# Kernel tuning notes

Hardware: AMD Instinct MI355X
Metric: run time of the kernel (lower is better)

## Reference

```python
import jax, jax.numpy as jnp
import numpy as np

HID = 256
BATCH = 16384
L_K = 4


def _mixture(lst, Ws):
    # lst: [B, 4, H] candidate tensors; Ws: [H] scoring vector (Linear(H,1,bias=False))
    scores = jnp.einsum('bkh,h->bk', lst, Ws)            # [B, 4]
    w = jax.nn.softmax(scores, axis=-1)                  # softmax over the l=4 candidates
    out = jnp.einsum('bk,bkh->bh', w, lst)               # [B, H] mixture
    s = scores.sum(axis=0)                               # [4] summed over batch
    idx = jnp.argmax(s).astype(jnp.int32)                # routing decision
    ss = jnp.sort(s)
    margin = ss[-1] - ss[-2]                             # top-2 margin
    return out, idx, margin


def setup_inputs() -> dict:
    key = jax.random.key(0)
    ks = jax.random.split(key, 6)
    bound = 1.0 / np.sqrt(HID)
    x = jax.random.normal(ks[0], (BATCH, 1, HID), dtype=jnp.float32)
    h = jax.random.normal(ks[1], (BATCH, 1, HID), dtype=jnp.float32)
    L = jax.random.uniform(ks[2], (L_K, HID, HID), dtype=jnp.float32, minval=-bound, maxval=bound)
    R = jax.random.uniform(ks[3], (L_K, HID, HID), dtype=jnp.float32, minval=-bound, maxval=bound)
    # k=3 slots are initialized to identity / zero bias in the torch module
    L = L.at[3].set(jnp.eye(HID, dtype=jnp.float32))
    R = R.at[3].set(jnp.eye(HID, dtype=jnp.float32))
    b = jnp.zeros((L_K, HID), dtype=jnp.float32)
    Ws = jax.random.normal(ks[4], (HID,), dtype=jnp.float32) * bound
    return {'x': x, 'h': h, 'L': L, 'R': R, 'b': b, 'Ws': Ws}


def reference(x, h, L, R, b, Ws):
    x2 = x[:, 0, :]  # [B, H]
    h2 = h[:, 0, :]  # [B, H]

    z1 = jax.nn.sigmoid(x2 @ L[0] + h2 @ R[0] + b[0])
    r = jax.nn.sigmoid(x2 @ L[1] + h2 @ R[1] + b[1])
    z2 = jax.nn.sigmoid(x2 @ L[0] + h2 @ R[0] + b[0])  # identical expression in the source

    def lin(A, Bv):
        # candidate set: A @ L[k] + Bv @ R[k] + b[k] for k in 0..3 -> [B, 4, H]
        return jnp.einsum('bh,khd->bkd', A, L) + jnp.einsum('bh,khd->bkd', Bv, R) + b[None]

    rh, i1, m1 = _mixture(lin(h2, r), Ws)
    h_tilde, i2, m2 = _mixture(lin(x2, rh), Ws)

    omz_cand = 1.0 - (jnp.einsum('bh,khd->bkd', z1, R) + b[None])
    oneMinusZ1, i3, m3 = _mixture(omz_cand, Ws)

    zh_cand = jnp.einsum('bh,khd->bkd', h_tilde, L) * jnp.einsum('bh,khd->bkd', oneMinusZ1, R) + b[None]
    zh_tilde, i4, m4 = _mixture(zh_cand, Ws)

    z2h_cand = jnp.einsum('bh,khd->bkd', h2, L) * jnp.einsum('bh,khd->bkd', z2, R) + b[None]
    z2h, i5, m5 = _mixture(z2h_cand, Ws)

    h_next, i6, m6 = _mixture(lin(zh_tilde, z2h), Ws)

    G_structure = jnp.concatenate([
        jnp.array([0, 1, 0], dtype=jnp.int32),
        jnp.stack([i1, i2, i3, i4, i5, i6]),
    ])
    G_node = jnp.stack([z1, r, z2, rh, h_tilde, oneMinusZ1, zh_tilde, z2h, h_next], axis=1)  # [B, 9, H]
    margins = jnp.stack([m1, m2, m3, m4, m5, m6])
    return h_next[:, None, :], G_structure, G_node, margins
```

## Files before the change

### kernel.cpp

```cpp
#include <hip/hip_runtime.h>

typedef __bf16 bf16_t;
typedef bf16_t bf16x8 __attribute__((ext_vector_type(8)));
typedef float f32x4 __attribute__((ext_vector_type(4)));

#define BATCH 16384
#define HID 256

__device__ __forceinline__ ushort f2b(float f) {
  union { float f; unsigned u; } v; v.f = f;
  unsigned u = v.u;
  unsigned r = (u + 0x7fffu + ((u >> 16) & 1u)) >> 16;
  return (ushort)r;
}
__device__ __forceinline__ float b2f(ushort u) {
  union { unsigned u; float f; } v; v.u = ((unsigned)u) << 16; return v.f;
}
__device__ __forceinline__ void loadbf4(const ushort* __restrict__ p, float* o) {
  uint2 q = *(const uint2*)p;
  o[0] = b2f((ushort)(q.x & 0xffffu));
  o[1] = b2f((ushort)(q.x >> 16));
  o[2] = b2f((ushort)(q.y & 0xffffu));
  o[3] = b2f((ushort)(q.y >> 16));
}
__device__ __forceinline__ uint2 packbf4(const float* v) {
  uint2 q;
  q.x = (unsigned)f2b(v[0]) | ((unsigned)f2b(v[1]) << 16);
  q.y = (unsigned)f2b(v[2]) | ((unsigned)f2b(v[3]) << 16);
  return q;
}

__global__ __launch_bounds__(256)
void f2b2_kernel(const float* __restrict__ a, const float* __restrict__ b,
                 ushort* __restrict__ oa, ushort* __restrict__ ob) {
  int bid = blockIdx.x;
  const float* in = (bid < 4096) ? a : b;
  ushort* out     = (bid < 4096) ? oa : ob;
  int t = (bid & 4095) * 256 + threadIdx.x;
  float4 v = *(const float4*)(in + (size_t)t * 4);
  float q[4] = {v.x, v.y, v.z, v.w};
  *(uint2*)(out + (size_t)t * 4) = packbf4(q);
}

__global__ __launch_bounds__(256)
void wt2_kernel(const float* __restrict__ L, const float* __restrict__ R,
                ushort* __restrict__ Lt, ushort* __restrict__ Rt) {
  int bid = blockIdx.x;
  const float* W = (bid < 1024) ? L : R;
  ushort* Wt     = (bid < 1024) ? Lt : Rt;
  int idx = (bid & 1023) * 256 + threadIdx.x;
  int c = idx >> 8, hh = idx & 255;
  int ks = c >> 8, d = c & 255;
  Wt[idx] = f2b(W[ks * 65536 + hh * 256 + d]);
}

__global__ __launch_bounds__(256, 2)
void gemm_kernel(const ushort* __restrict__ A, const ushort* __restrict__ Wt,
                 ushort* __restrict__ P, int N) {
  __shared__ __align__(16) ushort As[2][128 * 64];
  __shared__ __align__(16) ushort Bs[2][128 * 64];

  const int tid  = threadIdx.x;
  const int lane = tid & 63;
  const int wave = tid >> 6;

  const int nwg = gridDim.x;
  const int q   = nwg >> 3;
  const int bid = blockIdx.x;
  const int id2 = (bid & 7) * q + (bid >> 3);
  const int nx  = N >> 7;
  const int lnx = (nx == 8) ? 3 : 2;
  const int cn  = id2 & (nx - 1);
  const int cm  = id2 >> lnx;
  const int bm  = cm * 128;
  const int bn  = cn * 128;

  const int wm   = (wave >> 1) * 64;
  const int wn   = (wave & 1) * 64;
  const int row  = lane & 15;
  const int quad = lane >> 4;

  const int r_s = lane >> 3;
  const int g_s = lane & 7;
  const int gsw = g_s ^ r_s;

  f32x4 acc[4][4] = {};

#define STAGE(buf, t)                                                              \
  {                                                                                \
    const int k0 = (t) * 64;                                                       \
    for (int i = 0; i < 4; ++i) {                                                  \
      const int ci = wave * 4 + i;                                                 \
      const int r  = ci * 8 + r_s;                                                 \
      const ushort* srcA = A  + (size_t)(bm + r) * 256 + k0 + gsw * 8;             \
      const ushort* srcB = Wt + (size_t)(bn + r) * 256 + k0 + gsw * 8;             \
      __builtin_amdgcn_global_load_lds(                                            \
          (const __attribute__((address_space(1))) void*)srcA,                     \
          (__attribute__((address_space(3))) void*)&As[buf][ci * 512], 16, 0, 0);  \
      __builtin_amdgcn_global_load_lds(                                            \
          (const __attribute__((address_space(1))) void*)srcB,                     \
          (__attribute__((address_space(3))) void*)&Bs[buf][ci * 512], 16, 0, 0);  \
    }                                                                              \
  }

#define COMPUTE(buf)                                                               \
  {                                                                                \
    bf16x8 af[2][4], bf[2][4];                                                     \
    for (int kk = 0; kk < 2; ++kk)                                                 \
      for (int t = 0; t < 4; ++t) {                                                \
        const int ar = wm + t * 16 + row;                                          \
        const int ga = (kk * 4 + quad) ^ (ar & 7);                                 \
        af[kk][t] = *(const bf16x8*)&As[buf][ar * 64 + ga * 8];                    \
        const int br = wn + t * 16 + row;                                          \
        const int gb = (kk * 4 + quad) ^ (br & 7);                                 \
        bf[kk][t] = *(const bf16x8*)&Bs[buf][br * 64 + gb * 8];                    \
      }                                                                            \
    for (int kk = 0; kk < 2; ++kk)                                                 \
      for (int ti = 0; ti < 4; ++ti)                                               \
        for (int tj = 0; tj < 4; ++tj)                                             \
          acc[ti][tj] = __builtin_amdgcn_mfma_f32_16x16x32_bf16(                   \
              af[kk][ti], bf[kk][tj], acc[ti][tj], 0, 0, 0);                       \
  }

  STAGE(0, 0);
  __syncthreads();
  COMPUTE(0);
  STAGE(1, 1);
  __syncthreads();
  COMPUTE(1);
  STAGE(0, 2);
  __syncthreads();
  COMPUTE(0);
  STAGE(1, 3);
  __syncthreads();
  COMPUTE(1);
#undef STAGE
#undef COMPUTE

  for (int ti = 0; ti < 4; ++ti)
    for (int tj = 0; tj < 4; ++tj)
      for (int r2 = 0; r2 < 4; ++r2) {
        int gm = bm + wm + ti * 16 + quad * 4 + r2;
        int gn = bn + wn + tj * 16 + row;
        P[(size_t)gm * N + gn] = f2b(acc[ti][tj][r2]);
      }
}

__global__ __launch_bounds__(256)
void sig_kernel(const ushort* __restrict__ P0, const ushort* __restrict__ P2,
                const float* __restrict__ bias, float* __restrict__ gnode,
                ushort* __restrict__ z1b, ushort* __restrict__ rb) {
  int t = blockIdx.x * 256 + threadIdx.x;
  int b = t >> 6;
  int d0 = (t & 63) * 4;
  float xl[4], hr[4], z[4], r[4];
  loadbf4(P0 + (size_t)b * 1024 + d0, xl);
  loadbf4(P2 + (size_t)b * 512 + d0, hr);
  float4 bb = *(const float4*)(bias + d0);
  float bbb[4] = {bb.x, bb.y, bb.z, bb.w};
  for (int i = 0; i < 4; ++i) z[i] = 1.0f / (1.0f + expf(-(xl[i] + hr[i] + bbb[i])));
  size_t g = (size_t)b * 2304 + d0;
  for (int i = 0; i < 4; ++i) { gnode[g + i] = z[i]; gnode[g + 512 + i] = z[i]; }
  *(uint2*)(z1b + (size_t)b * 256 + d0) = packbf4(z);
  loadbf4(P0 + (size_t)b * 1024 + 256 + d0, xl);
  loadbf4(P2 + (size_t)b * 512 + 256 + d0, hr);
  float4 b1 = *(const float4*)(bias + 256 + d0);
  float b1b[4] = {b1.x, b1.y, b1.z, b1.w};
  for (int i = 0; i < 4; ++i) r[i] = 1.0f / (1.0f + expf(-(xl[i] + hr[i] + b1b[i])));
  for (int i = 0; i < 4; ++i) gnode[g + 256 + i] = r[i];
  *(uint2*)(rb + (size_t)b * 256 + d0) = packbf4(r);
}

__global__ __launch_bounds__(256)
void mix_kernel(const ushort* __restrict__ P1, const ushort* __restrict__ P2,
                const float* __restrict__ bias, const float* __restrict__ Ws,
                float* __restrict__ gnode, ushort* __restrict__ actout,
                float* __restrict__ hnext, float* __restrict__ part, int mode) {
  const int tid  = threadIdx.x;
  const int wave = tid >> 6;
  const int lane = tid & 63;
  const int row  = blockIdx.x * 4 + wave;
  const int d0   = lane * 4;
  float c[4][4];
  float sp[4];
  float4 w4 = *(const float4*)(Ws + d0);
  float ws4[4] = {w4.x, w4.y, w4.z, w4.w};
  for (int k = 0; k < 4; ++k) {
    float p1[4];
    loadbf4(P1 + (size_t)row * 1024 + k * 256 + d0, p1);
    float4 bb = *(const float4*)(bias + k * 256 + d0);
    float bv[4] = {bb.x, bb.y, bb.z, bb.w};
    float v[4];
    if (mode == 0) {
      float p2[4];
      loadbf4(P2 + (size_t)row * 1024 + k * 256 + d0, p2);
      for (int i = 0; i < 4; ++i) v[i] = p1[i] + p2[i] + bv[i];
    } else if (mode == 1) {
      for (int i = 0; i < 4; ++i) v[i] = 1.0f - (p1[i] + bv[i]);
    } else {
      float p2[4];
      loadbf4(P2 + (size_t)row * 1024 + k * 256 + d0, p2);
      for (int i = 0; i < 4; ++i) v[i] = p1[i] * p2[i] + bv[i];
    }
    float s = 0.f;
    for (int i = 0; i < 4; ++i) { c[k][i] = v[i]; s += v[i] * ws4[i]; }
    sp[k] = s;
  }
  for (int m = 1; m < 64; m <<= 1)
    for (int k = 0; k < 4; ++k) sp[k] += __shfl_xor(sp[k], m, 64);
  float mx = fmaxf(fmaxf(sp[0], sp[1]), fmaxf(sp[2], sp[3]));
  float e0 = expf(sp[0] - mx), e1 = expf(sp[1] - mx), e2 = expf(sp[2] - mx), e3 = expf(sp[3] - mx);
  float inv = 1.0f / (e0 + e1 + e2 + e3);
  float w0 = e0 * inv, w1 = e1 * inv, w2 = e2 * inv, w3 = e3 * inv;
  float o[4];
  for (int i = 0; i < 4; ++i) o[i] = w0 * c[0][i] + w1 * c[1][i] + w2 * c[2][i] + w3 * c[3][i];
  size_t g = (size_t)row * 2304 + d0;
  for (int i = 0; i < 4; ++i) gnode[g + i] = o[i];
  if (actout) *(uint2*)(actout + (size_t)row * 256 + d0) = packbf4(o);
  if (hnext) { float4 ov = {o[0], o[1], o[2], o[3]}; *(float4*)(hnext + (size_t)row * 256 + d0) = ov; }
  __shared__ float sred[4][4];
  if (lane == 0) for (int k = 0; k < 4; ++k) sred[wave][k] = sp[k];
  __syncthreads();
  if (tid < 4)
    part[blockIdx.x * 4 + tid] = sred[0][tid] + sred[1][tid] + sred[2][tid] + sred[3][tid];
}

__global__ __launch_bounds__(256)
void fin_kernel(const float* __restrict__ part, float* __restrict__ gs,
                float* __restrict__ margins) {
  __shared__ float red[256][4];
  __shared__ float sfin[6][4];
  int tid = threadIdx.x;
  for (int si = 0; si < 6; ++si) {
    float a[4] = {0.f, 0.f, 0.f, 0.f};
    for (int i = 0; i < 16; ++i) {
      const float* p = part + ((size_t)si * 4096 + tid + 256 * i) * 4;
      for (int k = 0; k < 4; ++k) a[k] += p[k];
    }
    for (int k = 0; k < 4; ++k) red[tid][k] = a[k];
    __syncthreads();
    for (int st = 128; st >= 1; st >>= 1) {
      if (tid < st) for (int k = 0; k < 4; ++k) red[tid][k] += red[tid + st][k];
      __syncthreads();
    }
    if (tid == 0) for (int k = 0; k < 4; ++k) sfin[si][k] = red[0][k];
    __syncthreads();
  }
  if (tid == 0) {
    gs[0] = 0.f; gs[1] = 1.f; gs[2] = 0.f;
    for (int si = 0; si < 6; ++si) {
      float s[4] = {sfin[si][0], sfin[si][1], sfin[si][2], sfin[si][3]};
      int idx = 0; float best = s[0];
      for (int k = 1; k < 4; ++k) if (s[k] > best) { best = s[k]; idx = k; }
      float second = -3.4e38f;
      for (int k = 0; k < 4; ++k) if (k != idx) second = fmaxf(second, s[k]);
      gs[3 + si] = (float)idx;
      margins[si] = best - second;
    }
  }
}

extern "C" void kernel_launch(void* const* d_in, const int* in_sizes, int n_in,
                              void* d_out, int out_size, void* d_ws, size_t ws_size,
                              hipStream_t stream) {
  const float* x    = (const float*)d_in[0];
  const float* h    = (const float*)d_in[1];
  const float* L    = (const float*)d_in[2];
  const float* R    = (const float*)d_in[3];
  const float* bias = (const float*)d_in[4];
  const float* Ws   = (const float*)d_in[5];

  float* out        = (float*)d_out;
  float* out_hnext  = out;
  float* out_gs     = out + 4194304;
  float* out_gnode  = out + 4194313;
  float* out_marg   = out + 41943049;

  ushort* P0   = (ushort*)d_ws;
  ushort* P1   = P0 + (size_t)BATCH * 1024;
  ushort* P2   = P1 + (size_t)BATCH * 1024;
  ushort* x2b  = P2 + (size_t)BATCH * 1024;
  ushort* h2b  = x2b + (size_t)BATCH * HID;
  ushort* z1b  = h2b + (size_t)BATCH * HID;
  ushort* rb   = z1b + (size_t)BATCH * HID;
  ushort* rhb  = rb  + (size_t)BATCH * HID;
  ushort* htb  = rhb + (size_t)BATCH * HID;
  ushort* omzb = htb + (size_t)BATCH * HID;
  ushort* ztb  = omzb + (size_t)BATCH * HID;
  ushort* z2hb = ztb + (size_t)BATCH * HID;
  ushort* Lt   = z2hb + (size_t)BATCH * HID;
  ushort* Rt   = Lt + 1024 * 256;
  float*  part = (float*)(Rt + 1024 * 256);

  f2b2_kernel<<<8192, 256, 0, stream>>>(x, h, x2b, h2b);
  wt2_kernel<<<2048, 256, 0, stream>>>(L, R, Lt, Rt);

  gemm_kernel<<<1024, 256, 0, stream>>>(x2b, Lt, P0, 1024);
  gemm_kernel<<<1024, 256, 0, stream>>>(h2b, Lt, P1, 1024);
  gemm_kernel<<< 512, 256, 0, stream>>>(h2b, Rt, P2, 512);

  sig_kernel<<<4096, 256, 0, stream>>>(P0, P2, bias, out_gnode, z1b, rb);

  gemm_kernel<<<1024, 256, 0, stream>>>(rb, Rt, P2, 1024);
  mix_kernel<<<4096, 256, 0, stream>>>(P1, P2, bias, Ws, out_gnode + 3 * 256, rhb,
                                       nullptr, part + 0 * 4096 * 4, 0);
  gemm_kernel<<<1024, 256, 0, stream>>>(rhb, Rt, P2, 1024);
  mix_kernel<<<4096, 256, 0, stream>>>(P0, P2, bias, Ws, out_gnode + 4 * 256, htb,
                                       nullptr, part + 1 * 4096 * 4, 0);
  gemm_kernel<<<1024, 256, 0, stream>>>(z1b, Rt, P0, 1024);
  mix_kernel<<<4096, 256, 0, stream>>>(P0, P0, bias, Ws, out_gnode + 5 * 256, omzb,
                                       nullptr, part + 2 * 4096 * 4, 1);
  mix_kernel<<<4096, 256, 0, stream>>>(P1, P0, bias, Ws, out_gnode + 7 * 256, z2hb,
                                       nullptr, part + 4 * 4096 * 4, 2);
  gemm_kernel<<<1024, 256, 0, stream>>>(htb, Lt, P1, 1024);
  gemm_kernel<<<1024, 256, 0, stream>>>(omzb, Rt, P2, 1024);
  mix_kernel<<<4096, 256, 0, stream>>>(P1, P2, bias, Ws, out_gnode + 6 * 256, ztb,
                                       nullptr, part + 3 * 4096 * 4, 2);
  gemm_kernel<<<1024, 256, 0, stream>>>(ztb, Lt, P0, 1024);
  gemm_kernel<<<1024, 256, 0, stream>>>(z2hb, Rt, P1, 1024);
  mix_kernel<<<4096, 256, 0, stream>>>(P0, P1, bias, Ws, out_gnode + 8 * 256, nullptr,
                                       out_hnext, part + 5 * 4096 * 4, 0);
  fin_kernel<<<1, 256, 0, stream>>>(part, out_gs, out_marg);
}
```

Baseline: 488.7 us.

## Fuse paired GEMMs via K-concatenation and batch independent jobs per launch

GEMMs of the form A@L + B@R now run as a single K=512 GEMM that walks two A/B operand pairs. Bias add and the sigmoid gate computation move into the GEMM epilogue, which removes sig_kernel. Independent GEMMs and mixture kernels are packed into shared launches through job structs. Together these cut launch count and the intermediate bf16 P-buffer traffic, since the sum-of-two-products tensors are no longer written and re-read. The costs are a scalar, uncoalesced epilogue with expf and bias loads per element, and runtime branching on job fields.

After: 604.3 us. 23.7% more time.

```diff
diff --git a/kernel.cpp b/kernel.cpp
--- a/kernel.cpp
+++ b/kernel.cpp
@@ -54,26 +54,37 @@
   Wt[idx] = f2b(W[ks * 65536 + hh * 256 + d]);
 }
 
+struct GJob {
+  const ushort* A1; const ushort* A2;
+  const ushort* B1; const ushort* B2;
+  ushort* out;
+  const float* bias;
+  float* gnode; ushort* z1b; ushort* rb;
+  int nx;
+  int epi;
+  int nblocks;
+};
+
 __global__ __launch_bounds__(256, 2)
-void gemm_kernel(const ushort* __restrict__ A, const ushort* __restrict__ Wt,
-                 ushort* __restrict__ P, int N) {
+void fgemm_kernel(GJob j0, GJob j1, int split) {
   __shared__ __align__(16) ushort As[2][128 * 64];
   __shared__ __align__(16) ushort Bs[2][128 * 64];
+
+  const int bid  = blockIdx.x;
+  const GJob j   = (bid < split) ? j0 : j1;
+  const int lbid = (bid < split) ? bid : bid - split;
 
   const int tid  = threadIdx.x;
   const int lane = tid & 63;
   const int wave = tid >> 6;
 
-  const int nwg = gridDim.x;
-  const int q   = nwg >> 3;
-  const int bid = blockIdx.x;
-  const int id2 = (bid & 7) * q + (bid >> 3);
-  const int nx  = N >> 7;
-  const int lnx = (nx == 8) ? 3 : 2;
-  const int cn  = id2 & (nx - 1);
-  const int cm  = id2 >> lnx;
-  const int bm  = cm * 128;
-  const int bn  = cn * 128;
+  const int q   = j.nblocks >> 3;
+  const int id2 = (lbid & 7) * q + (lbid >> 3);
+  int cn, cm;
+  if (j.nx == 8) { cn = id2 & 7; cm = id2 >> 3; }
+  else           { cn = id2 & 3; cm = id2 >> 2; }
+  const int bm = cm * 128;
+  const int bn = cn * 128;
 
   const int wm   = (wave >> 1) * 64;
   const int wn   = (wave & 1) * 64;
@@ -86,100 +97,109 @@
 
   f32x4 acc[4][4] = {};
 
-#define STAGE(buf, t)                                                              \
+#define STAGE(buf, kt)                                                             \
   {                                                                                \
-    const int k0 = (t) * 64;                                                       \
-    for (int i = 0; i < 4; ++i) {                                                  \
-      const int ci = wave * 4 + i;                                                 \
+    const int bufs = (buf);                                                        \
+    const int kts  = (kt);                                                         \
+    const ushort* Ab = (kts < 4) ? j.A1 : j.A2;                                    \
+    const ushort* Bb = (kts < 4) ? j.B1 : j.B2;                                    \
+    const int k0 = (kts & 3) * 64;                                                 \
+    for (int i_s = 0; i_s < 4; ++i_s) {                                            \
+      const int ci = wave * 4 + i_s;                                               \
       const int r  = ci * 8 + r_s;                                                 \
-      const ushort* srcA = A  + (size_t)(bm + r) * 256 + k0 + gsw * 8;             \
-      const ushort* srcB = Wt + (size_t)(bn + r) * 256 + k0 + gsw * 8;             \
       __builtin_amdgcn_global_load_lds(                                            \
-          (const __attribute__((address_space(1))) void*)srcA,                     \
-          (__attribute__((address_space(3))) void*)&As[buf][ci * 512], 16, 0, 0);  \
+          (const __attribute__((address_space(1))) void*)(Ab + (size_t)(bm + r) * 256 + k0 + gsw * 8), \
+          (__attribute__((address_space(3))) void*)&As[bufs][ci * 512], 16, 0, 0); \
       __builtin_amdgcn_global_load_lds(                                            \
-          (const __attribute__((address_space(1))) void*)srcB,                     \
-          (__attribute__((address_space(3))) void*)&Bs[buf][ci * 512], 16, 0, 0);  \
+          (const __attribute__((address_space(1))) void*)(Bb + (size_t)(bn + r) * 256 + k0 + gsw * 8), \
+          (__attribute__((address_space(3))) void*)&Bs[bufs][ci * 512], 16, 0, 0); \
     }                                                                              \
   }
 
 #define COMPUTE(buf)                                                               \
   {                                                                                \
-    bf16x8 af[2][4], bf[2][4];                                                     \
-    for (int kk = 0; kk < 2; ++kk)                                                 \
-      for (int t = 0; t < 4; ++t) {                                                \
-        const int ar = wm + t * 16 + row;                                          \
-        const int ga = (kk * 4 + quad) ^ (ar & 7);                                 \
-        af[kk][t] = *(const bf16x8*)&As[buf][ar * 64 + ga * 8];                    \
-        const int br = wn + t * 16 + row;                                          \
-        const int gb = (kk * 4 + quad) ^ (br & 7);                                 \
-        bf[kk][t] = *(const bf16x8*)&Bs[buf][br * 64 + gb * 8];                    \
+    const int bufc = (buf);                                                        \
+    bf16x8 af[2][4], bfr[2][4];                                                    \
+    for (int kk_c = 0; kk_c < 2; ++kk_c)                                           \
+      for (int fr_c = 0; fr_c < 4; ++fr_c) {                                       \
+        const int ar = wm + fr_c * 16 + row;                                       \
+        const int ga = (kk_c * 4 + quad) ^ (ar & 7);                               \
+        af[kk_c][fr_c] = *(const bf16x8*)&As[bufc][ar * 64 + ga * 8];              \
+        const int br = wn + fr_c * 16 + row;                                       \
+        const int gb = (kk_c * 4 + quad) ^ (br & 7);                               \
+        bfr[kk_c][fr_c] = *(const bf16x8*)&Bs[bufc][br * 64 + gb * 8];             \
       }                                                                            \
-    for (int kk = 0; kk < 2; ++kk)                                                 \
+    for (int kk_c = 0; kk_c < 2; ++kk_c)                                           \
       for (int ti = 0; ti < 4; ++ti)                                               \
         for (int tj = 0; tj < 4; ++tj)                                             \
           acc[ti][tj] = __builtin_amdgcn_mfma_f32_16x16x32_bf16(                   \
-              af[kk][ti], bf[kk][tj], acc[ti][tj], 0, 0, 0);                       \
+              af[kk_c][ti], bfr[kk_c][tj], acc[ti][tj], 0, 0, 0);                  \
   }
 
   STAGE(0, 0);
   __syncthreads();
-  COMPUTE(0);
-  STAGE(1, 1);
-  __syncthreads();
-  COMPUTE(1);
-  STAGE(0, 2);
-  __syncthreads();
-  COMPUTE(0);
-  STAGE(1, 3);
-  __syncthreads();
-  COMPUTE(1);
+  if (j.A2 != nullptr) {
+#pragma unroll
+    for (int t = 0; t < 8; ++t) {
+      if (t < 7) STAGE((t + 1) & 1, t + 1);
+      COMPUTE(t & 1);
+      if (t < 7) __syncthreads();
+    }
+  } else {
+#pragma unroll
+    for (int t = 0; t < 4; ++t) {
+      if (t < 3) STAGE((t + 1) & 1, t + 1);
+      COMPUTE(t & 1);
+      if (t < 3) __syncthreads();
+    }
+  }
 #undef STAGE
 #undef COMPUTE
 
+  const int N = j.nx * 128;
   for (int ti = 0; ti < 4; ++ti)
     for (int tj = 0; tj < 4; ++tj)
       for (int r2 = 0; r2 < 4; ++r2) {
         int gm = bm + wm + ti * 16 + quad * 4 + r2;
         int gn = bn + wn + tj * 16 + row;
-        P[(size_t)gm * N + gn] = f2b(acc[ti][tj][r2]);
+        float v = acc[ti][tj][r2];
+        if (j.epi == 0) {
+          j.out[(size_t)gm * N + gn] = f2b(v);
+        } else if (j.epi == 1) {
+          j.out[(size_t)gm * N + gn] = f2b(v + j.bias[gn]);
+        } else {
+          float s = 1.0f / (1.0f + expf(-(v + j.bias[gn])));
+          size_t g = (size_t)gm * 2304;
+          if (gn < 256) {
+            j.gnode[g + gn] = s;
+            j.gnode[g + 512 + gn] = s;
+            j.z1b[(size_t)gm * 256 + gn] = f2b(s);
+          } else {
+            int d = gn - 256;
+            j.gnode[g + 256 + d] = s;
+            j.rb[(size_t)gm * 256 + d] = f2b(s);
+          }
+        }
       }
 }
 
+struct MixJob {
+  const ushort* P1; const ushort* P2;
+  float* gnode; ushort* act; float* hnext; float* part;
+  int mode;
+};
+
 __global__ __launch_bounds__(256)
-void sig_kernel(const ushort* __restrict__ P0, const ushort* __restrict__ P2,
-                const float* __restrict__ bias, float* __restrict__ gnode,
-                ushort* __restrict__ z1b, ushort* __restrict__ rb) {
-  int t = blockIdx.x * 256 + threadIdx.x;
-  int b = t >> 6;
-  int d0 = (t & 63) * 4;
-  float xl[4], hr[4], z[4], r[4];
-  loadbf4(P0 + (size_t)b * 1024 + d0, xl);
-  loadbf4(P2 + (size_t)b * 512 + d0, hr);
-  float4 bb = *(const float4*)(bias + d0);
-  float bbb[4] = {bb.x, bb.y, bb.z, bb.w};
-  for (int i = 0; i < 4; ++i) z[i] = 1.0f / (1.0f + expf(-(xl[i] + hr[i] + bbb[i])));
-  size_t g = (size_t)b * 2304 + d0;
-  for (int i = 0; i < 4; ++i) { gnode[g + i] = z[i]; gnode[g + 512 + i] = z[i]; }
-  *(uint2*)(z1b + (size_t)b * 256 + d0) = packbf4(z);
-  loadbf4(P0 + (size_t)b * 1024 + 256 + d0, xl);
-  loadbf4(P2 + (size_t)b * 512 + 256 + d0, hr);
-  float4 b1 = *(const float4*)(bias + 256 + d0);
-  float b1b[4] = {b1.x, b1.y, b1.z, b1.w};
-  for (int i = 0; i < 4; ++i) r[i] = 1.0f / (1.0f + expf(-(xl[i] + hr[i] + b1b[i])));
-  for (int i = 0; i < 4; ++i) gnode[g + 256 + i] = r[i];
-  *(uint2*)(rb + (size_t)b * 256 + d0) = packbf4(r);
-}
-
-__global__ __launch_bounds__(256)
-void mix_kernel(const ushort* __restrict__ P1, const ushort* __restrict__ P2,
-                const float* __restrict__ bias, const float* __restrict__ Ws,
-                float* __restrict__ gnode, ushort* __restrict__ actout,
-                float* __restrict__ hnext, float* __restrict__ part, int mode) {
+void mixN_kernel(MixJob j0, MixJob j1, MixJob j2, const float* __restrict__ bias,
+                 const float* __restrict__ Ws) {
+  const int jb = blockIdx.x >> 12;
+  const MixJob j = (jb == 0) ? j0 : (jb == 1) ? j1 : j2;
+  const int lb = blockIdx.x & 4095;
+
   const int tid  = threadIdx.x;
   const int wave = tid >> 6;
   const int lane = tid & 63;
-  const int row  = blockIdx.x * 4 + wave;
+  const int row  = lb * 4 + wave;
   const int d0   = lane * 4;
   float c[4][4];
   float sp[4];
@@ -187,20 +207,20 @@
   float ws4[4] = {w4.x, w4.y, w4.z, w4.w};
   for (int k = 0; k < 4; ++k) {
     float p1[4];
-    loadbf4(P1 + (size_t)row * 1024 + k * 256 + d0, p1);
-    float4 bb = *(const float4*)(bias + k * 256 + d0);
-    float bv[4] = {bb.x, bb.y, bb.z, bb.w};
+    loadbf4(j.P1 + (size_t)row * 1024 + k * 256 + d0, p1);
     float v[4];
-    if (mode == 0) {
-      float p2[4];
-      loadbf4(P2 + (size_t)row * 1024 + k * 256 + d0, p2);
-      for (int i = 0; i < 4; ++i) v[i] = p1[i] + p2[i] + bv[i];
-    } else if (mode == 1) {
-      for (int i = 0; i < 4; ++i) v[i] = 1.0f - (p1[i] + bv[i]);
+    if (j.mode == 3) {
+      for (int i = 0; i < 4; ++i) v[i] = p1[i];
     } else {
-      float p2[4];
-      loadbf4(P2 + (size_t)row * 1024 + k * 256 + d0, p2);
-      for (int i = 0; i < 4; ++i) v[i] = p1[i] * p2[i] + bv[i];
+      float4 bb = *(const float4*)(bias + k * 256 + d0);
+      float bv[4] = {bb.x, bb.y, bb.z, bb.w};
+      if (j.mode == 1) {
+        for (int i = 0; i < 4; ++i) v[i] = 1.0f - (p1[i] + bv[i]);
+      } else {
+        float p2[4];
+        loadbf4(j.P2 + (size_t)row * 1024 + k * 256 + d0, p2);
+        for (int i = 0; i < 4; ++i) v[i] = p1[i] * p2[i] + bv[i];
+      }
     }
     float s = 0.f;
     for (int i = 0; i < 4; ++i) { c[k][i] = v[i]; s += v[i] * ws4[i]; }
@@ -215,14 +235,14 @@
   float o[4];
   for (int i = 0; i < 4; ++i) o[i] = w0 * c[0][i] + w1 * c[1][i] + w2 * c[2][i] + w3 * c[3][i];
   size_t g = (size_t)row * 2304 + d0;
-  for (int i = 0; i < 4; ++i) gnode[g + i] = o[i];
-  if (actout) *(uint2*)(actout + (size_t)row * 256 + d0) = packbf4(o);
-  if (hnext) { float4 ov = {o[0], o[1], o[2], o[3]}; *(float4*)(hnext + (size_t)row * 256 + d0) = ov; }
+  for (int i = 0; i < 4; ++i) j.gnode[g + i] = o[i];
+  if (j.act) *(uint2*)(j.act + (size_t)row * 256 + d0) = packbf4(o);
+  if (j.hnext) { float4 ov = {o[0], o[1], o[2], o[3]}; *(float4*)(j.hnext + (size_t)row * 256 + d0) = ov; }
   __shared__ float sred[4][4];
   if (lane == 0) for (int k = 0; k < 4; ++k) sred[wave][k] = sp[k];
   __syncthreads();
   if (tid < 4)
-    part[blockIdx.x * 4 + tid] = sred[0][tid] + sred[1][tid] + sred[2][tid] + sred[3][tid];
+    j.part[lb * 4 + tid] = sred[0][tid] + sred[1][tid] + sred[2][tid] + sred[3][tid];
 }
 
 __global__ __launch_bounds__(256)
@@ -295,30 +315,51 @@
   f2b2_kernel<<<8192, 256, 0, stream>>>(x, h, x2b, h2b);
   wt2_kernel<<<2048, 256, 0, stream>>>(L, R, Lt, Rt);
 
-  gemm_kernel<<<1024, 256, 0, stream>>>(x2b, Lt, P0, 1024);
-  gemm_kernel<<<1024, 256, 0, stream>>>(h2b, Lt, P1, 1024);
-  gemm_kernel<<< 512, 256, 0, stream>>>(h2b, Rt, P2, 512);
-
-  sig_kernel<<<4096, 256, 0, stream>>>(P0, P2, bias, out_gnode, z1b, rb);
-
-  gemm_kernel<<<1024, 256, 0, stream>>>(rb, Rt, P2, 1024);
-  mix_kernel<<<4096, 256, 0, stream>>>(P1, P2, bias, Ws, out_gnode + 3 * 256, rhb,
-                                       nullptr, part + 0 * 4096 * 4, 0);
-  gemm_kernel<<<1024, 256, 0, stream>>>(rhb, Rt, P2, 1024);
-  mix_kernel<<<4096, 256, 0, stream>>>(P0, P2, bias, Ws, out_gnode + 4 * 256, htb,
-                                       nullptr, part + 1 * 4096 * 4, 0);
-  gemm_kernel<<<1024, 256, 0, stream>>>(z1b, Rt, P0, 1024);
-  mix_kernel<<<4096, 256, 0, stream>>>(P0, P0, bias, Ws, out_gnode + 5 * 256, omzb,
-                                       nullptr, part + 2 * 4096 * 4, 1);
-  mix_kernel<<<4096, 256, 0, stream>>>(P1, P0, bias, Ws, out_gnode + 7 * 256, z2hb,
-                                       nullptr, part + 4 * 4096 * 4, 2);
-  gemm_kernel<<<1024, 256, 0, stream>>>(htb, Lt, P1, 1024);
-  gemm_kernel<<<1024, 256, 0, stream>>>(omzb, Rt, P2, 1024);
-  mix_kernel<<<4096, 256, 0, stream>>>(P1, P2, bias, Ws, out_gnode + 6 * 256, ztb,
-                                       nullptr, part + 3 * 4096 * 4, 2);
-  gemm_kernel<<<1024, 256, 0, stream>>>(ztb, Lt, P0, 1024);
-  gemm_kernel<<<1024, 256, 0, stream>>>(z2hb, Rt, P1, 1024);
-  mix_kernel<<<4096, 256, 0, stream>>>(P0, P1, bias, Ws, out_gnode + 8 * 256, nullptr,
-                                       out_hnext, part + 5 * 4096 * 4, 0);
+  GJob jz = {};
+
+  {
+    GJob a = {x2b, h2b, Lt, Rt, nullptr, bias, out_gnode, z1b, rb, 4, 2, 512};
+    GJob b = {h2b, nullptr, Lt, nullptr, P0, nullptr, nullptr, nullptr, nullptr, 8, 0, 1024};
+    fgemm_kernel<<<1536, 256, 0, stream>>>(a, b, 512);
+  }
+  {
+    GJob a = {h2b, rb, Lt, Rt, P1, bias, nullptr, nullptr, nullptr, 8, 1, 1024};
+    GJob b = {z1b, nullptr, Rt, nullptr, P2, nullptr, nullptr, nullptr, nullptr, 8, 0, 1024};
+    fgemm_kernel<<<2048, 256, 0, stream>>>(a, b, 1024);
+  }
+  {
+    MixJob m0 = {P1, nullptr, out_gnode + 3 * 256, rhb,  nullptr, part + 0 * 16384, 3};
+    MixJob m1 = {P2, nullptr, out_gnode + 5 * 256, omzb, nullptr, part + 2 * 16384, 1};
+    MixJob m2 = {P0, P2,      out_gnode + 7 * 256, z2hb, nullptr, part + 4 * 16384, 2};
+    mixN_kernel<<<12288, 256, 0, stream>>>(m0, m1, m2, bias, Ws);
+  }
+  {
+    GJob a = {x2b, rhb, Lt, Rt, P0, bias, nullptr, nullptr, nullptr, 8, 1, 1024};
+    fgemm_kernel<<<1024, 256, 0, stream>>>(a, jz, 1024);
+  }
+  {
+    MixJob m0 = {P0, nullptr, out_gnode + 4 * 256, htb, nullptr, part + 1 * 16384, 3};
+    MixJob mz = m0;
+    mixN_kernel<<<4096, 256, 0, stream>>>(m0, mz, mz, bias, Ws);
+  }
+  {
+    GJob a = {htb,  nullptr, Lt, nullptr, P1, nullptr, nullptr, nullptr, nullptr, 8, 0, 1024};
+    GJob b = {omzb, nullptr, Rt, nullptr, P2, nullptr, nullptr, nullptr, nullptr, 8, 0, 1024};
+    fgemm_kernel<<<2048, 256, 0, stream>>>(a, b, 1024);
+  }
+  {
+    MixJob m0 = {P1, P2, out_gnode + 6 * 256, ztb, nullptr, part + 3 * 16384, 2};
+    MixJob mz = m0;
+    mixN_kernel<<<4096, 256, 0, stream>>>(m0, mz, mz, bias, Ws);
+  }
+  {
+    GJob a = {ztb, z2hb, Lt, Rt, P0, bias, nullptr, nullptr, nullptr, 8, 1, 1024};
+    fgemm_kernel<<<1024, 256, 0, stream>>>(a, jz, 1024);
+  }
+  {
+    MixJob m0 = {P0, nullptr, out_gnode + 8 * 256, nullptr, out_hnext, part + 5 * 16384, 3};
+    MixJob mz = m0;
+    mixN_kernel<<<4096, 256, 0, stream>>>(m0, mz, mz, bias, Ws);
+  }
   fin_kernel<<<1, 256, 0, stream>>>(part, out_gs, out_marg);
 }
```
